# Kernel tuning notes

Measured on AMD Instinct MI355X. Metric: run time of the kernel, lower is better.

Reference implementation:

```python
import jax, jax.numpy as jnp
import numpy as np

HEADS = 4
DIM_HEAD = 32


def setup_inputs() -> dict:
    key = jax.random.key(0)
    k1, k2, k3 = jax.random.split(key, 3)
    b, dim, h, w = 16, 256, 64, 64
    hidden = HEADS * DIM_HEAD  # 128
    x = jax.random.normal(k1, (b, dim, h, w), dtype=jnp.float32)
    # 1x1 convs are just channel matmuls; store kernels as 2D matrices.
    W_qkv = jax.random.normal(k2, (3 * hidden, dim), dtype=jnp.float32) * 0.02
    W_out = jax.random.normal(k3, (dim, hidden), dtype=jnp.float32) * 0.02
    b_out = jnp.zeros((dim,), dtype=jnp.float32)
    return {"x": x, "W_qkv": W_qkv, "W_out": W_out, "b_out": b_out}


def reference(x, W_qkv, W_out, b_out):
    b, c, h, w = x.shape
    n = h * w
    # 1x1 conv: (b, 3*hidden, h, w) -> view (b, 3, heads, dim_head, n)
    qkv = jnp.einsum('bchw,oc->bohw', x, W_qkv)
    qkv = qkv.reshape(b, 3, HEADS, DIM_HEAD, n)
    q, k, v = qkv[:, 0], qkv[:, 1], qkv[:, 2]  # each (b, heads, dim_head, n)
    k = jax.nn.softmax(k, axis=-1)
    # context: (b, heads, dim_head, dim_head)
    context = jnp.einsum('bhdn,bhen->bhde', k, v)
    # out: (b, heads, dim_head, n)
    out = jnp.einsum('bhde,bhen->bhdn', context, q)
    out = out.reshape(b, HEADS * DIM_HEAD, h, w)
    # to_out 1x1 conv with bias
    y = jnp.einsum('bchw,oc->bohw', out, W_out) + b_out[None, :, None, None]
    return y
```

## Files before the change

### kernel.cpp

```cpp
#include <hip/hip_runtime.h>

typedef __attribute__((ext_vector_type(8))) short short8;
typedef __attribute__((ext_vector_type(4))) float f32x4;
typedef unsigned short u16;
typedef unsigned int u32;


__device__ __forceinline__ u16 f2bf(float f) {
    u32 x = __float_as_uint(f);
    u32 r = (x + 0x7fffu + ((x >> 16) & 1u)) >> 16;
    return (u16)r;
}

typedef __attribute__((address_space(1))) u32 as1_u32;
typedef __attribute__((address_space(3))) u32 as3_u32;
__device__ __forceinline__ void gload16(const void* g, void* l) {
    __builtin_amdgcn_global_load_lds((as1_u32*)g, (as3_u32*)l, 16, 0, 0);
}

__global__ __launch_bounds__(512) void k_fused(const float* __restrict__ x,
                                               const float* __restrict__ Wqkv,
                                               u16* __restrict__ xT,
                                               float* __restrict__ part,
                                               float* __restrict__ denp) {
    __shared__ alignas(16) char smem[104448];
    u16* sB = (u16*)smem;
    u16* sA = (u16*)(smem + 67584);
    u16* Pl = (u16*)smem;
    u16* Vl = (u16*)(smem + 34816);
    float* dpart = (float*)(smem + 69632);

    int t = threadIdx.x;
    int nt = blockIdx.x, b = blockIdx.y;
    int n0 = nt * 128;
    int lane = t & 63, wv = t >> 6, l16 = lane & 15, lq = lane >> 4;
    int wr = wv >> 1, wc = wv & 1;

    for (int i = 0; i < 16; i++) {
        int qi = i * 512 + t;
        int cl = qi >> 5;
        int nq = (qi & 31) * 4;
        float4 v = *reinterpret_cast<const float4*>(x + ((size_t)(b * 256 + cl) * 4096 + n0 + nq));
        float vv[4] = {v.x, v.y, v.z, v.w};
#pragma unroll
        for (int j = 0; j < 4; j++) {
            int n = nq + j;
            int cs = cl ^ (((n >> 3) & 7) << 3);
            sB[n * 264 + cs] = f2bf(vv[j]);
        }
    }
    __syncthreads();
    for (int i = 0; i < 8; i++) {
        int wi = i * 512 + t;
        int nl = wi >> 5;
        int cg = (wi & 31) * 8;
        int cs = cg ^ (((nl >> 3) & 7) << 3);
        uint4 vals = *reinterpret_cast<const uint4*>(&sB[nl * 264 + cs]);
        *reinterpret_cast<uint4*>(xT + ((size_t)(b * 4096 + n0 + nl) * 256 + cg)) = vals;
    }

    f32x4 acc[4][4];
#pragma unroll
    for (int i = 0; i < 4; i++)
#pragma unroll
        for (int j = 0; j < 4; j++) acc[i][j] = (f32x4){0.f, 0.f, 0.f, 0.f};

    const float* Wsrc = Wqkv + 128 * 256;
    for (int kc = 0; kc < 4; kc++) {
        __syncthreads();
#pragma unroll
        for (int q = 0; q < 8; q++) {
            int fi = q * 512 + t;
            int row = fi >> 4, cq = (fi & 15) * 4;
            float4 w = *reinterpret_cast<const float4*>(Wsrc + (size_t)row * 256 + kc * 64 + cq);
            u32 w0 = (u32)f2bf(w.x) | ((u32)f2bf(w.y) << 16);
            u32 w1 = (u32)f2bf(w.z) | ((u32)f2bf(w.w) << 16);
            uint2 o = {w0, w1};
            *reinterpret_cast<uint2*>(&sA[row * 72 + cq]) = o;
        }
        __syncthreads();
#pragma unroll
        for (int ks = 0; ks < 2; ks++) {
            int colA = ks * 32 + lq * 8;
            int colB = kc * 64 + ks * 32 + lq * 8;
            short8 af[4], bfr[4];
#pragma unroll
            for (int i = 0; i < 4; i++)
                af[i] = *reinterpret_cast<const short8*>(&sA[(wr * 64 + i * 16 + l16) * 72 + colA]);
#pragma unroll
            for (int j = 0; j < 4; j++) {
                int n = wc * 64 + j * 16 + l16;
                int cs = colB ^ (((n >> 3) & 7) << 3);
                bfr[j] = *reinterpret_cast<const short8*>(&sB[n * 264 + cs]);
            }
#pragma unroll
            for (int i = 0; i < 4; i++)
#pragma unroll
                for (int j = 0; j < 4; j++)
                    acc[i][j] = __builtin_amdgcn_mfma_f32_16x16x32_bf16(af[i], bfr[j], acc[i][j], 0, 0, 0);
        }
    }
    __syncthreads();

    if (wr < 2) {
#pragma unroll
        for (int i = 0; i < 4; i++) {
            int rbase = wr * 64 + i * 16 + lq * 4;
            float srow[4] = {0.f, 0.f, 0.f, 0.f};
#pragma unroll
            for (int j = 0; j < 4; j++) {
                int n = wc * 64 + j * 16 + l16;
#pragma unroll
                for (int rr = 0; rr < 4; rr++) {
                    float e = __expf(acc[i][j][rr]);
                    Pl[(rbase + rr) * 136 + n] = f2bf(e);
                    srow[rr] += e;
                }
            }
#pragma unroll
            for (int rr = 0; rr < 4; rr++) {
                float s = srow[rr];
                s += __shfl_xor(s, 1, 64); s += __shfl_xor(s, 2, 64);
                s += __shfl_xor(s, 4, 64); s += __shfl_xor(s, 8, 64);
                if (l16 == 0) dpart[(rbase + rr) * 2 + wc] = s;
            }
        }
    } else {
#pragma unroll
        for (int i = 0; i < 4; i++) {
            int rbase = (wr - 2) * 64 + i * 16 + lq * 4;
#pragma unroll
            for (int j = 0; j < 4; j++) {
                int n = wc * 64 + j * 16 + l16;
#pragma unroll
                for (int rr = 0; rr < 4; rr++)
                    Vl[(rbase + rr) * 136 + n] = f2bf(acc[i][j][rr]);
            }
        }
    }
    __syncthreads();

    int h = wv >> 1, eh = wv & 1;
    f32x4 a2[2];
    a2[0] = (f32x4){0.f, 0.f, 0.f, 0.f};
    a2[1] = (f32x4){0.f, 0.f, 0.f, 0.f};
#pragma unroll
    for (int kk = 0; kk < 4; kk++) {
        int col = kk * 32 + lq * 8;
        short8 bfr = *reinterpret_cast<const short8*>(&Vl[(h * 32 + eh * 16 + l16) * 136 + col]);
#pragma unroll
        for (int i = 0; i < 2; i++) {
            short8 af = *reinterpret_cast<const short8*>(&Pl[(h * 32 + i * 16 + l16) * 136 + col]);
            a2[i] = __builtin_amdgcn_mfma_f32_16x16x32_bf16(af, bfr, a2[i], 0, 0, 0);
        }
    }
    float* pp = part + ((size_t)(b * 32 + nt) * 4 + h) * 1024;
#pragma unroll
    for (int i = 0; i < 2; i++)
#pragma unroll
        for (int rr = 0; rr < 4; rr++)
            pp[(i * 16 + lq * 4 + rr) * 32 + eh * 16 + l16] = a2[i][rr];

    if (t < 128)
        denp[((size_t)b * 128 + t) * 32 + nt] = dpart[t * 2] + dpart[t * 2 + 1];
}

__global__ __launch_bounds__(256) void k_red(const float* __restrict__ part,
                                             const float* __restrict__ denp,
                                             float* __restrict__ C) {
    __shared__ float invd[32];
    int bh = blockIdx.x;
    int b = bh >> 2, h = bh & 3;
    int t = threadIdx.x;
    if (t < 32) {
        const float* dp = denp + ((size_t)b * 128 + h * 32 + t) * 32;
        float s = 0.f;
#pragma unroll
        for (int nt = 0; nt < 32; nt++) s += dp[nt];
        invd[t] = 1.0f / s;
    }
    __syncthreads();
    int de0 = t * 4;
    float a0 = 0.f, a1 = 0.f, a2 = 0.f, a3 = 0.f;
#pragma unroll 8
    for (int nt = 0; nt < 32; nt++) {
        f32x4 v = *reinterpret_cast<const f32x4*>(part + ((size_t)(b * 32 + nt) * 4 + h) * 1024 + de0);
        a0 += v[0]; a1 += v[1]; a2 += v[2]; a3 += v[3];
    }
    float iv = invd[de0 >> 5];
    f32x4 o = {a0 * iv, a1 * iv, a2 * iv, a3 * iv};
    *reinterpret_cast<f32x4*>(C + (size_t)bh * 1024 + de0) = o;
}

__global__ __launch_bounds__(256) void k_G(const float* __restrict__ C,
                                           const float* __restrict__ Wout,
                                           const float* __restrict__ Wqkv,
                                           u16* __restrict__ Gb) {
    __shared__ float Cs[4096];
    __shared__ float Us[2048];
    int b = blockIdx.x, ot = blockIdx.y, t = threadIdx.x;
    int o0 = ot * 16;
#pragma unroll
    for (int q = 0; q < 16; q++) {
        int idx = q * 256 + t;
        Cs[idx] = C[(size_t)b * 4096 + idx];
    }
    __syncthreads();
#pragma unroll
    for (int q = 0; q < 8; q++) {
        int idx = q * 256 + t;
        int ol = idx >> 7, he = idx & 127;
        int h = he >> 5, e = he & 31;
        const float* wrow = Wout + (o0 + ol) * 128 + h * 32;
        const float* crow = &Cs[h * 1024 + e];
        float a = 0.f;
#pragma unroll
        for (int d = 0; d < 32; d++) a += wrow[d] * crow[d * 32];
        Us[idx] = a;
    }
    __syncthreads();
    int ol = t >> 4, c0 = (t & 15) * 16;
    float acc[16];
#pragma unroll
    for (int cc = 0; cc < 16; cc++) acc[cc] = 0.f;
    const float* Ur = &Us[ol * 128];
#pragma unroll 4
    for (int he = 0; he < 128; he++) {
        float u = Ur[he];
        const float4* wq = reinterpret_cast<const float4*>(Wqkv + he * 256 + c0);
#pragma unroll
        for (int q4 = 0; q4 < 4; q4++) {
            float4 w = wq[q4];
            acc[q4 * 4 + 0] += u * w.x;
            acc[q4 * 4 + 1] += u * w.y;
            acc[q4 * 4 + 2] += u * w.z;
            acc[q4 * 4 + 3] += u * w.w;
        }
    }
    alignas(16) u16 ob[16];
#pragma unroll
    for (int cc = 0; cc < 16; cc++) ob[cc] = f2bf(acc[cc]);
    u16* dst = Gb + (size_t)(b * 256 + o0 + ol) * 256 + c0;
    *reinterpret_cast<uint4*>(dst) = *reinterpret_cast<const uint4*>(ob);
    *reinterpret_cast<uint4*>(dst + 8) = *reinterpret_cast<const uint4*>(ob + 8);
}

__global__ __launch_bounds__(256) void k_y(const u16* __restrict__ Gb,
                                           const u16* __restrict__ xT,
                                           const float* __restrict__ bout,
                                           float* __restrict__ y) {
    __shared__ alignas(16) u16 sA[128 * 64];
    __shared__ alignas(16) u16 sB[128 * 64];
    int t = threadIdx.x;
    int mt = blockIdx.x, n0 = blockIdx.y * 128, b = blockIdx.z;
    int m0 = mt * 128;
    int lane = t & 63, wv = t >> 6, l16 = lane & 15, lq = lane >> 4;
    int wr = wv >> 1, wc = wv & 1;
    int trow = t >> 3, tc8 = (t & 7) * 8;

    f32x4 acc[4][4];
#pragma unroll
    for (int i = 0; i < 4; i++)
#pragma unroll
        for (int j = 0; j < 4; j++) acc[i][j] = (f32x4){0.f, 0.f, 0.f, 0.f};

    const u16* Asrc = Gb + (size_t)(b * 256 + m0) * 256;
    const u16* Bsrc = xT + (size_t)(b * 4096 + n0) * 256;

    for (int kc = 0; kc < 4; kc++) {
        __syncthreads();
#pragma unroll
        for (int q = 0; q < 4; q++) {
            int row = q * 32 + trow;
            gload16(Asrc + (size_t)row * 256 + kc * 64 + tc8, &sA[row * 64 + tc8]);
            gload16(Bsrc + (size_t)row * 256 + kc * 64 + tc8, &sB[row * 64 + tc8]);
        }
        __syncthreads();
#pragma unroll
        for (int ks = 0; ks < 2; ks++) {
            int col = ks * 32 + lq * 8;
            short8 af[4], bfr[4];
#pragma unroll
            for (int i = 0; i < 4; i++)
                af[i] = *reinterpret_cast<const short8*>(&sA[(wr * 64 + i * 16 + l16) * 64 + col]);
#pragma unroll
            for (int j = 0; j < 4; j++)
                bfr[j] = *reinterpret_cast<const short8*>(&sB[(wc * 64 + j * 16 + l16) * 64 + col]);
#pragma unroll
            for (int i = 0; i < 4; i++)
#pragma unroll
                for (int j = 0; j < 4; j++)
                    acc[i][j] = __builtin_amdgcn_mfma_f32_16x16x32_bf16(af[i], bfr[j], acc[i][j], 0, 0, 0);
        }
    }
#pragma unroll
    for (int i = 0; i < 4; i++) {
        int obase = m0 + wr * 64 + i * 16 + lq * 4;
#pragma unroll
        for (int j = 0; j < 4; j++) {
            int n = n0 + wc * 64 + j * 16 + l16;
#pragma unroll
            for (int rr = 0; rr < 4; rr++) {
                int o = obase + rr;
                y[(size_t)(b * 256 + o) * 4096 + n] = acc[i][j][rr] + bout[o];
            }
        }
    }
}

extern "C" void kernel_launch(void* const* d_in, const int* in_sizes, int n_in,
                              void* d_out, int out_size, void* d_ws, size_t ws_size,
                              hipStream_t stream) {
    const float* x    = (const float*)d_in[0];
    const float* Wqkv = (const float*)d_in[1];
    const float* Wout = (const float*)d_in[2];
    const float* bout = (const float*)d_in[3];
    float* y = (float*)d_out;

    char* ws = (char*)d_ws;
    u16*   xT   = (u16*)(ws);
    float* part = (float*)(ws + 33554432);
    float* denp = (float*)(ws + 41943040);
    float* C    = (float*)(ws + 42205184);
    u16*   Gb   = (u16*)(ws + 42467328);

    k_fused<<<dim3(32, 16), 512, 0, stream>>>(x, Wqkv, xT, part, denp);
    k_red  <<<64, 256, 0, stream>>>(part, denp, C);
    k_G    <<<dim3(16, 16), 256, 0, stream>>>(C, Wout, Wqkv, Gb);
    k_y    <<<dim3(2, 32, 16), 256, 0, stream>>>(Gb, xT, bout, y);
}
```

Before: 193.5 us.

## Split transpose and weight conversion out of fused kernel, use async LDS loads

Moves the x-to-bf16 transpose into a dedicated high-parallelism kernel and pre-converts Wqkv to bf16 once, so the fused projection kernel streams bf16 tiles via global_load_lds instead of converting fp32 in registers. Shared memory in the fused kernel drops, allowing higher occupancy (launch bounds 512,4). k_G is split across two channel halves and reads bf16 weights. It adds two kernel launches and an extra round trip of xT through global memory before the fused kernel reads it back.

After: 175.0 us. -9.6%, faster.

```diff
diff --git a/kernel.cpp b/kernel.cpp
--- a/kernel.cpp
+++ b/kernel.cpp
@@ -11,6 +11,9 @@
     u32 r = (x + 0x7fffu + ((x >> 16) & 1u)) >> 16;
     return (u16)r;
 }
+__device__ __forceinline__ float bf2f(u16 h) {
+    return __uint_as_float(((u32)h) << 16);
+}
 
 typedef __attribute__((address_space(1))) u32 as1_u32;
 typedef __attribute__((address_space(3))) u32 as3_u32;
@@ -18,14 +21,51 @@
     __builtin_amdgcn_global_load_lds((as1_u32*)g, (as3_u32*)l, 16, 0, 0);
 }
 
-__global__ __launch_bounds__(512) void k_fused(const float* __restrict__ x,
-                                               const float* __restrict__ Wqkv,
-                                               u16* __restrict__ xT,
-                                               float* __restrict__ part,
-                                               float* __restrict__ denp) {
-    __shared__ alignas(16) char smem[104448];
-    u16* sB = (u16*)smem;
-    u16* sA = (u16*)(smem + 67584);
+__global__ __launch_bounds__(256) void k_convW(const float* __restrict__ W,
+                                               u16* __restrict__ Wb) {
+    int idx = blockIdx.x * 256 + threadIdx.x;
+    float4 v = *reinterpret_cast<const float4*>(W + idx * 4);
+    u32 w0 = (u32)f2bf(v.x) | ((u32)f2bf(v.y) << 16);
+    u32 w1 = (u32)f2bf(v.z) | ((u32)f2bf(v.w) << 16);
+    uint2 o = {w0, w1};
+    *reinterpret_cast<uint2*>(Wb + idx * 4) = o;
+}
+
+__global__ __launch_bounds__(256) void k_transpose(const float* __restrict__ x,
+                                                   u16* __restrict__ xT) {
+    __shared__ alignas(16) u16 tile[64 * 72];
+    int t = threadIdx.x;
+    int n0 = blockIdx.x * 64, c0 = blockIdx.y * 64, b = blockIdx.z;
+    int rr = t >> 4, nq = (t & 15) * 4;
+#pragma unroll
+    for (int i = 0; i < 4; i++) {
+        int cl = i * 16 + rr;
+        float4 v = *reinterpret_cast<const float4*>(x + ((size_t)(b * 256 + c0 + cl) * 4096 + n0 + nq));
+        u32 w0 = (u32)f2bf(v.x) | ((u32)f2bf(v.y) << 16);
+        u32 w1 = (u32)f2bf(v.z) | ((u32)f2bf(v.w) << 16);
+        uint2 o = {w0, w1};
+        *reinterpret_cast<uint2*>(&tile[cl * 72 + nq]) = o;
+    }
+    __syncthreads();
+    int r = t >> 3, c8 = (t & 7) * 8;
+#pragma unroll
+    for (int i = 0; i < 2; i++) {
+        int nl = i * 32 + r;
+        alignas(16) u16 vals[8];
+#pragma unroll
+        for (int j = 0; j < 8; j++) vals[j] = tile[(c8 + j) * 72 + nl];
+        *reinterpret_cast<uint4*>(xT + ((size_t)(b * 4096 + n0 + nl) * 256 + c0 + c8)) =
+            *reinterpret_cast<const uint4*>(vals);
+    }
+}
+
+__global__ __launch_bounds__(512, 4) void k_fused(const u16* __restrict__ xT,
+                                                  const u16* __restrict__ Wb,
+                                                  float* __restrict__ part,
+                                                  float* __restrict__ denp) {
+    __shared__ alignas(16) char smem[70656];
+    u16* sA = (u16*)smem;
+    u16* sB = (u16*)(smem + 32768);
     u16* Pl = (u16*)smem;
     u16* Vl = (u16*)(smem + 34816);
     float* dpart = (float*)(smem + 69632);
@@ -35,29 +75,7 @@
     int n0 = nt * 128;
     int lane = t & 63, wv = t >> 6, l16 = lane & 15, lq = lane >> 4;
     int wr = wv >> 1, wc = wv & 1;
-
-    for (int i = 0; i < 16; i++) {
-        int qi = i * 512 + t;
-        int cl = qi >> 5;
-        int nq = (qi & 31) * 4;
-        float4 v = *reinterpret_cast<const float4*>(x + ((size_t)(b * 256 + cl) * 4096 + n0 + nq));
-        float vv[4] = {v.x, v.y, v.z, v.w};
-#pragma unroll
-        for (int j = 0; j < 4; j++) {
-            int n = nq + j;
-            int cs = cl ^ (((n >> 3) & 7) << 3);
-            sB[n * 264 + cs] = f2bf(vv[j]);
-        }
-    }
-    __syncthreads();
-    for (int i = 0; i < 8; i++) {
-        int wi = i * 512 + t;
-        int nl = wi >> 5;
-        int cg = (wi & 31) * 8;
-        int cs = cg ^ (((nl >> 3) & 7) << 3);
-        uint4 vals = *reinterpret_cast<const uint4*>(&sB[nl * 264 + cs]);
-        *reinterpret_cast<uint4*>(xT + ((size_t)(b * 4096 + n0 + nl) * 256 + cg)) = vals;
-    }
+    int trow = t >> 3, tc8 = (t & 7) * 8;
 
     f32x4 acc[4][4];
 #pragma unroll
@@ -65,34 +83,32 @@
 #pragma unroll
         for (int j = 0; j < 4; j++) acc[i][j] = (f32x4){0.f, 0.f, 0.f, 0.f};
 
-    const float* Wsrc = Wqkv + 128 * 256;
+    const u16* Asrc = Wb + 128 * 256;
+    const u16* Bsrc = xT + (size_t)(b * 4096 + n0) * 256;
+
     for (int kc = 0; kc < 4; kc++) {
         __syncthreads();
 #pragma unroll
-        for (int q = 0; q < 8; q++) {
-            int fi = q * 512 + t;
-            int row = fi >> 4, cq = (fi & 15) * 4;
-            float4 w = *reinterpret_cast<const float4*>(Wsrc + (size_t)row * 256 + kc * 64 + cq);
-            u32 w0 = (u32)f2bf(w.x) | ((u32)f2bf(w.y) << 16);
-            u32 w1 = (u32)f2bf(w.z) | ((u32)f2bf(w.w) << 16);
-            uint2 o = {w0, w1};
-            *reinterpret_cast<uint2*>(&sA[row * 72 + cq]) = o;
+        for (int q = 0; q < 4; q++) {
+            int row = q * 64 + trow;
+            gload16(Asrc + (size_t)row * 256 + kc * 64 + tc8, &sA[row * 64 + tc8]);
+        }
+#pragma unroll
+        for (int q = 0; q < 2; q++) {
+            int row = q * 64 + trow;
+            gload16(Bsrc + (size_t)row * 256 + kc * 64 + tc8, &sB[row * 64 + tc8]);
         }
         __syncthreads();
 #pragma unroll
         for (int ks = 0; ks < 2; ks++) {
-            int colA = ks * 32 + lq * 8;
-            int colB = kc * 64 + ks * 32 + lq * 8;
+            int col = ks * 32 + lq * 8;
             short8 af[4], bfr[4];
 #pragma unroll
             for (int i = 0; i < 4; i++)
-                af[i] = *reinterpret_cast<const short8*>(&sA[(wr * 64 + i * 16 + l16) * 72 + colA]);
-#pragma unroll
-            for (int j = 0; j < 4; j++) {
-                int n = wc * 64 + j * 16 + l16;
-                int cs = colB ^ (((n >> 3) & 7) << 3);
-                bfr[j] = *reinterpret_cast<const short8*>(&sB[n * 264 + cs]);
-            }
+                af[i] = *reinterpret_cast<const short8*>(&sA[(wr * 64 + i * 16 + l16) * 64 + col]);
+#pragma unroll
+            for (int j = 0; j < 4; j++)
+                bfr[j] = *reinterpret_cast<const short8*>(&sB[(wc * 64 + j * 16 + l16) * 64 + col]);
 #pragma unroll
             for (int i = 0; i < 4; i++)
 #pragma unroll
@@ -194,11 +210,11 @@
 
 __global__ __launch_bounds__(256) void k_G(const float* __restrict__ C,
                                            const float* __restrict__ Wout,
-                                           const float* __restrict__ Wqkv,
+                                           const u16* __restrict__ Wb,
                                            u16* __restrict__ Gb) {
     __shared__ float Cs[4096];
     __shared__ float Us[2048];
-    int b = blockIdx.x, ot = blockIdx.y, t = threadIdx.x;
+    int b = blockIdx.x, ot = blockIdx.y, ch = blockIdx.z, t = threadIdx.x;
     int o0 = ot * 16;
 #pragma unroll
     for (int q = 0; q < 16; q++) {
@@ -219,30 +235,24 @@
         Us[idx] = a;
     }
     __syncthreads();
-    int ol = t >> 4, c0 = (t & 15) * 16;
-    float acc[16];
-#pragma unroll
-    for (int cc = 0; cc < 16; cc++) acc[cc] = 0.f;
+    int ol = t >> 4, c0 = ch * 128 + (t & 15) * 8;
+    float acc[8];
+#pragma unroll
+    for (int cc = 0; cc < 8; cc++) acc[cc] = 0.f;
     const float* Ur = &Us[ol * 128];
 #pragma unroll 4
     for (int he = 0; he < 128; he++) {
         float u = Ur[he];
-        const float4* wq = reinterpret_cast<const float4*>(Wqkv + he * 256 + c0);
-#pragma unroll
-        for (int q4 = 0; q4 < 4; q4++) {
-            float4 w = wq[q4];
-            acc[q4 * 4 + 0] += u * w.x;
-            acc[q4 * 4 + 1] += u * w.y;
-            acc[q4 * 4 + 2] += u * w.z;
-            acc[q4 * 4 + 3] += u * w.w;
-        }
-    }
-    alignas(16) u16 ob[16];
-#pragma unroll
-    for (int cc = 0; cc < 16; cc++) ob[cc] = f2bf(acc[cc]);
-    u16* dst = Gb + (size_t)(b * 256 + o0 + ol) * 256 + c0;
-    *reinterpret_cast<uint4*>(dst) = *reinterpret_cast<const uint4*>(ob);
-    *reinterpret_cast<uint4*>(dst + 8) = *reinterpret_cast<const uint4*>(ob + 8);
+        short8 w8 = *reinterpret_cast<const short8*>(Wb + he * 256 + c0);
+#pragma unroll
+        for (int e = 0; e < 8; e++)
+            acc[e] += u * bf2f((u16)w8[e]);
+    }
+    alignas(16) u16 ob[8];
+#pragma unroll
+    for (int cc = 0; cc < 8; cc++) ob[cc] = f2bf(acc[cc]);
+    *reinterpret_cast<uint4*>(Gb + (size_t)(b * 256 + o0 + ol) * 256 + c0) =
+        *reinterpret_cast<const uint4*>(ob);
 }
 
 __global__ __launch_bounds__(256) void k_y(const u16* __restrict__ Gb,
@@ -323,9 +333,12 @@
     float* denp = (float*)(ws + 41943040);
     float* C    = (float*)(ws + 42205184);
     u16*   Gb   = (u16*)(ws + 42467328);
-
-    k_fused<<<dim3(32, 16), 512, 0, stream>>>(x, Wqkv, xT, part, denp);
-    k_red  <<<64, 256, 0, stream>>>(part, denp, C);
-    k_G    <<<dim3(16, 16), 256, 0, stream>>>(C, Wout, Wqkv, Gb);
-    k_y    <<<dim3(2, 32, 16), 256, 0, stream>>>(Gb, xT, bout, y);
-}
+    u16*   Wb   = (u16*)(ws + 44564480);
+
+    k_convW    <<<96, 256, 0, stream>>>(Wqkv, Wb);
+    k_transpose<<<dim3(64, 4, 16), 256, 0, stream>>>(x, xT);
+    k_fused    <<<dim3(32, 16), 512, 0, stream>>>(xT, Wb, part, denp);
+    k_red      <<<64, 256, 0, stream>>>(part, denp, C);
+    k_G        <<<dim3(16, 16, 2), 256, 0, stream>>>(C, Wout, Wb, Gb);
+    k_y        <<<dim3(2, 32, 16), 256, 0, stream>>>(Gb, xT, bout, y);
+}
```
